# Optimization experiments

Hardware: AMD Instinct MI355X
Metric: run time of the kernel (lower is better)

Reference implementation:

```python
import jax, jax.numpy as jnp
import numpy as np

SCALE = 0.125  # 1/sqrt(d_k), d_k = 64


def setup_inputs() -> dict:
    key = jax.random.key(0)
    kq, kk, kv, kp = jax.random.split(key, 4)
    H, B, L, T, D = 16, 4, 1024, 1024, 64
    return {
        "query": jax.random.normal(kq, (H, B, L, D), dtype=jnp.float32),
        "key": jax.random.normal(kk, (H, B, T, D), dtype=jnp.float32),
        "value": jax.random.normal(kv, (H, B, T, D), dtype=jnp.float32),
        "prev_attention": jax.random.normal(kp, (H, B, L, T), dtype=jnp.float32),
    }


def reference(query, key, value, prev_attention):
    # scores: [h, b, l, t]
    scores = jnp.einsum("hblk,hbtk->hblt", query, key) * SCALE
    scores = scores + prev_attention
    attention = jax.nn.softmax(scores, axis=-1)
    # dropout disabled (rate 0.0) for deterministic reference
    output = jnp.einsum("hblt,hbtv->hblv", attention, value)
    return (output, attention)
```

## Files before the change

kernel.cpp:

```cpp
#include <hip/hip_runtime.h>

#define SCALE 0.125f

constexpr int L_ = 1024, T_ = 1024, D_ = 64, HB_ = 64;

using f32x4 = __attribute__((ext_vector_type(4))) float;
using half8 = __attribute__((ext_vector_type(8))) _Float16;
using half4 = __attribute__((ext_vector_type(4))) _Float16;

__global__ __launch_bounds__(256, 4) void zpass(
    const float* __restrict__ q, const float* __restrict__ kk,
    const float* __restrict__ prev, float* __restrict__ att,
    float* __restrict__ rz) {
  __shared__ __align__(16) _Float16 Ks[2][64][72];

  const int ltile = blockIdx.x, hb = blockIdx.y;
  const int tid = threadIdx.x;
  const int w = tid >> 6, l = tid & 63, l15 = l & 15, lg = l >> 4;
  const int qrow = ltile * 64 + w * 16 + l15;

  half8 qb[2];
  {
    const float* qp = q + ((size_t)hb * L_ + qrow) * D_ + lg * 8;
#pragma unroll
    for (int f = 0; f < 2; ++f)
#pragma unroll
      for (int e = 0; e < 8; ++e) qb[f][e] = (_Float16)qp[f * 32 + e];
  }

  const float* prow = prev + ((size_t)hb * L_ + qrow) * (size_t)T_;
  const float* kbase = kk + (size_t)hb * T_ * D_;
  _Float16* erow =
      (_Float16*)(att + ((size_t)hb * L_ + qrow) * (size_t)T_) + T_;

  const int sr = tid >> 2;
  const int sc = (tid & 3) * 16;

  float4 kreg[4];
  auto kload = [&](int t0) {
    const float* kp = kbase + (size_t)(t0 + sr) * D_ + sc;
#pragma unroll
    for (int p = 0; p < 4; ++p) kreg[p] = *(const float4*)(kp + p * 4);
  };
  auto kwrite = [&](int buf) {
#pragma unroll
    for (int p = 0; p < 4; ++p) {
      Ks[buf][sr][sc + p * 4 + 0] = (_Float16)kreg[p].x;
      Ks[buf][sr][sc + p * 4 + 1] = (_Float16)kreg[p].y;
      Ks[buf][sr][sc + p * 4 + 2] = (_Float16)kreg[p].z;
      Ks[buf][sr][sc + p * 4 + 3] = (_Float16)kreg[p].w;
    }
  };

  f32x4 pb[3][4];
  auto pload = [&](int c, int s) {
#pragma unroll
    for (int nt = 0; nt < 4; ++nt)
      pb[s][nt] = *(const f32x4*)(prow + c * 64 + nt * 16 + lg * 4);
  };

  kload(0);
  kwrite(0);
  pload(0, 0);
  pload(1, 1);

  float zsum = 0.f;

#pragma unroll
  for (int c = 0; c < 16; ++c) {
    const int cur = c & 1;
    if (c < 15) kload((c + 1) * 64);
    if (c < 14) pload(c + 2, (c + 2) % 3);
    __syncthreads();

#pragma unroll
    for (int nt = 0; nt < 4; ++nt) {
      half8 ka0 = *(const half8*)&Ks[cur][nt * 16 + l15][lg * 8];
      half8 ka1 = *(const half8*)&Ks[cur][nt * 16 + l15][32 + lg * 8];
      f32x4 acc = {0.f, 0.f, 0.f, 0.f};
      acc = __builtin_amdgcn_mfma_f32_16x16x32_f16(ka0, qb[0], acc, 0, 0, 0);
      acc = __builtin_amdgcn_mfma_f32_16x16x32_f16(ka1, qb[1], acc, 0, 0, 0);

      f32x4 pv = pb[c % 3][nt];
      float e0 = __expf(acc[0] * SCALE + pv[0]);
      float e1 = __expf(acc[1] * SCALE + pv[1]);
      float e2 = __expf(acc[2] * SCALE + pv[2]);
      float e3 = __expf(acc[3] * SCALE + pv[3]);
      zsum += (e0 + e1) + (e2 + e3);
      half4 ev;
      ev[0] = (_Float16)e0; ev[1] = (_Float16)e1;
      ev[2] = (_Float16)e2; ev[3] = (_Float16)e3;
      *(half4*)(erow + c * 64 + nt * 16 + lg * 4) = ev;
    }

    if (c < 15) kwrite(cur ^ 1);
  }

  zsum += __shfl_xor(zsum, 16, 64);
  zsum += __shfl_xor(zsum, 32, 64);
  if (lg == 0) rz[(size_t)hb * L_ + qrow] = 1.0f / zsum;
}

__global__ __launch_bounds__(256, 4) void pvpass(
    const float* __restrict__ vv, const float* __restrict__ rz,
    float* __restrict__ out, float* __restrict__ att) {
  __shared__ __align__(16) _Float16 Vt[2][64][72];

  const int ltile = blockIdx.x, hb = blockIdx.y;
  const int tid = threadIdx.x;
  const int w = tid >> 6, l = tid & 63, l15 = l & 15, lg = l >> 4;
  const int qrow = ltile * 64 + w * 16 + l15;

  const float rzq = rz[(size_t)hb * L_ + qrow];
  float* arow = att + ((size_t)hb * L_ + qrow) * (size_t)T_;
  const _Float16* erow = (const _Float16*)arow + T_;

  const float* vbase = vv + (size_t)hb * T_ * D_;
  const int sr = tid >> 2;
  const int dj = (tid & 3) * 4;

  float4 sv[4];
  auto stage_load = [&](int t0) {
    const float* vp = vbase + (size_t)(t0 + sr) * D_;
#pragma unroll
    for (int p = 0; p < 4; ++p) sv[p] = *(const float4*)(vp + p * 16 + dj);
  };
  auto stage_write = [&](int buf) {
#pragma unroll
    for (int p = 0; p < 4; ++p) {
      Vt[buf][p * 16 + dj + 0][sr] = (_Float16)sv[p].x;
      Vt[buf][p * 16 + dj + 1][sr] = (_Float16)sv[p].y;
      Vt[buf][p * 16 + dj + 2][sr] = (_Float16)sv[p].z;
      Vt[buf][p * 16 + dj + 3][sr] = (_Float16)sv[p].w;
    }
  };

  half8 eb[2][2];
  auto load_e = [&](int c, int buf) {
    eb[buf][0] = *(const half8*)(erow + c * 64 + lg * 8);
    eb[buf][1] = *(const half8*)(erow + c * 64 + 32 + lg * 8);
  };

  stage_load(0);
  stage_write(0);
  load_e(0, 0);

  f32x4 oacc[4];
#pragma unroll
  for (int nd = 0; nd < 4; ++nd) oacc[nd] = (f32x4){0.f, 0.f, 0.f, 0.f};

#pragma unroll
  for (int c = 0; c < 16; ++c) {
    __syncthreads();
    const int buf = c & 1;
    if (c < 15) {
      stage_load((c + 1) * 64);
      load_e(c + 1, (c + 1) & 1);
    }

    half8 af[2];
#pragma unroll
    for (int ks = 0; ks < 2; ++ks) {
      half8 ef = eb[buf][ks];
      f32x4 s0, s1;
#pragma unroll
      for (int e = 0; e < 4; ++e) {
        float v0 = (float)ef[e] * rzq;
        float v1 = (float)ef[4 + e] * rzq;
        s0[e] = v0; s1[e] = v1;
        af[ks][e] = (_Float16)v0;
        af[ks][4 + e] = (_Float16)v1;
      }
      *(f32x4*)(arow + c * 64 + ks * 32 + lg * 8) = s0;
      *(f32x4*)(arow + c * 64 + ks * 32 + lg * 8 + 4) = s1;
    }

#pragma unroll
    for (int ks = 0; ks < 2; ++ks)
#pragma unroll
      for (int nd = 0; nd < 4; ++nd) {
        half8 vb = *(const half8*)&Vt[buf][nd * 16 + l15][ks * 32 + lg * 8];
        oacc[nd] =
            __builtin_amdgcn_mfma_f32_16x16x32_f16(af[ks], vb, oacc[nd], 0, 0, 0);
      }

    if (c < 15) stage_write(buf ^ 1);
  }

  float* outw =
      out + ((size_t)hb * L_ + ltile * 64 + w * 16 + lg * 4) * (size_t)D_;
#pragma unroll
  for (int nd = 0; nd < 4; ++nd)
#pragma unroll
    for (int i = 0; i < 4; ++i)
      outw[(size_t)i * D_ + nd * 16 + l15] = oacc[nd][i];
}

extern "C" void kernel_launch(void* const* d_in, const int* in_sizes, int n_in,
                              void* d_out, int out_size, void* d_ws,
                              size_t ws_size, hipStream_t stream) {
  const float* q    = (const float*)d_in[0];
  const float* k    = (const float*)d_in[1];
  const float* v    = (const float*)d_in[2];
  const float* prev = (const float*)d_in[3];

  float* out = (float*)d_out;
  float* att = out + (size_t)HB_ * L_ * D_;
  float* rz  = (float*)d_ws;

  dim3 grid(L_ / 64, HB_);
  zpass<<<grid, 256, 0, stream>>>(q, k, prev, att, rz);
  pvpass<<<grid, 256, 0, stream>>>(v, rz, out, att);
}
```

Baseline: 254.8 us.

## Fuse score and PV passes into one kernel keeping exp values in LDS

Merges the two kernels into one. Unnormalized exp scores for a 32-row query tile are kept in 64KB of shared memory instead of being written as fp16 into the attention output buffer and read back. K and V are staged through a single swizzled LDS region, with each pair of waves splitting the key dimension and a final reduction across waves. This removes the global round trip of the intermediate exponentials and the row-sum workspace. In exchange it uses 80KB of LDS per block, which lowers occupancy, adds more barriers, and doubles K/V reloads because the query tile is smaller.

```diff
diff --git a/kernel.cpp b/kernel.cpp
--- a/kernel.cpp
+++ b/kernel.cpp
@@ -2,22 +2,37 @@
 
 #define SCALE 0.125f
 
-constexpr int L_ = 1024, T_ = 1024, D_ = 64, HB_ = 64;
+constexpr int L_ = 1024, T_ = 1024, D_ = 64, HB_ = 64, QB = 32;
 
 using f32x4 = __attribute__((ext_vector_type(4))) float;
 using half8 = __attribute__((ext_vector_type(8))) _Float16;
 using half4 = __attribute__((ext_vector_type(4))) _Float16;
 
-__global__ __launch_bounds__(256, 4) void zpass(
+__global__ __launch_bounds__(256, 2) void attn_fused(
     const float* __restrict__ q, const float* __restrict__ kk,
-    const float* __restrict__ prev, float* __restrict__ att,
-    float* __restrict__ rz) {
-  __shared__ __align__(16) _Float16 Ks[2][64][72];
-
-  const int ltile = blockIdx.x, hb = blockIdx.y;
+    const float* __restrict__ vv, const float* __restrict__ prev,
+    float* __restrict__ out, float* __restrict__ att) {
+  __shared__ __align__(16) unsigned char smem[81920];
+  unsigned char* Elb = smem;
+  unsigned char* KVb = smem + 65536;
+
+  const int ltile = blockIdx.x;
+  const int hb    = blockIdx.y;
   const int tid = threadIdx.x;
   const int w = tid >> 6, l = tid & 63, l15 = l & 15, lg = l >> 4;
-  const int qrow = ltile * 64 + w * 16 + l15;
+  const int rt = w >> 1, th = w & 1;
+  const int qloc = rt * 16 + l15;
+  const int qrow = ltile * QB + qloc;
+
+  auto elp = [&](int qq, int t) {
+    return Elb + qq * 2048 + (((unsigned)t * 2) ^ (((unsigned)qq & 7) << 4));
+  };
+  auto kp_ = [&](int row, int dbyte) {
+    return KVb + row * 128 + ((unsigned)dbyte ^ (((unsigned)row & 7) << 4));
+  };
+  auto vp_ = [&](int d, int tbyte) {
+    return KVb + d * 256 + ((unsigned)tbyte ^ (((unsigned)d & 7) << 4));
+  };
 
   half8 qb[2];
   {
@@ -28,60 +43,70 @@
       for (int e = 0; e < 8; ++e) qb[f][e] = (_Float16)qp[f * 32 + e];
   }
 
-  const float* prow = prev + ((size_t)hb * L_ + qrow) * (size_t)T_;
   const float* kbase = kk + (size_t)hb * T_ * D_;
-  _Float16* erow =
-      (_Float16*)(att + ((size_t)hb * L_ + qrow) * (size_t)T_) + T_;
-
-  const int sr = tid >> 2;
-  const int sc = (tid & 3) * 16;
-
-  float4 kreg[4];
-  auto kload = [&](int t0) {
-    const float* kp = kbase + (size_t)(t0 + sr) * D_ + sc;
-#pragma unroll
-    for (int p = 0; p < 4; ++p) kreg[p] = *(const float4*)(kp + p * 4);
-  };
-  auto kwrite = [&](int buf) {
-#pragma unroll
-    for (int p = 0; p < 4; ++p) {
-      Ks[buf][sr][sc + p * 4 + 0] = (_Float16)kreg[p].x;
-      Ks[buf][sr][sc + p * 4 + 1] = (_Float16)kreg[p].y;
-      Ks[buf][sr][sc + p * 4 + 2] = (_Float16)kreg[p].z;
-      Ks[buf][sr][sc + p * 4 + 3] = (_Float16)kreg[p].w;
-    }
-  };
-
-  f32x4 pb[3][4];
+  const float* vbase = vv + (size_t)hb * T_ * D_;
+  const float* prow  = prev + ((size_t)hb * L_ + qrow) * (size_t)T_;
+
+  const int sr = tid >> 1;
+  const int sh = (tid & 1) * 32;
+  float4 kreg[8];
+  auto gload = [&](const float* base, int c) {
+    const float* p = base + (size_t)(c * 128 + sr) * D_ + sh;
+#pragma unroll
+    for (int i = 0; i < 8; ++i) kreg[i] = *(const float4*)(p + i * 4);
+  };
+  auto kwrite = [&]() {
+#pragma unroll
+    for (int j = 0; j < 4; ++j) {
+      const float* f = (const float*)&kreg[j * 2];
+      half8 hv;
+#pragma unroll
+      for (int e = 0; e < 8; ++e) hv[e] = (_Float16)f[e];
+      *(half8*)kp_(sr, (sh + j * 8) * 2) = hv;
+    }
+  };
+  auto vwrite = [&]() {
+    const float* f = (const float*)kreg;
+#pragma unroll
+    for (int e = 0; e < 32; ++e)
+      *(_Float16*)vp_(sh + e, sr * 2) = (_Float16)f[e];
+  };
+
+  f32x4 pbuf[3][4];
   auto pload = [&](int c, int s) {
 #pragma unroll
     for (int nt = 0; nt < 4; ++nt)
-      pb[s][nt] = *(const f32x4*)(prow + c * 64 + nt * 16 + lg * 4);
-  };
-
-  kload(0);
-  kwrite(0);
+      pbuf[s][nt] =
+          *(const f32x4*)(prow + c * 128 + th * 64 + nt * 16 + lg * 4);
+  };
+
+  gload(kbase, 0);
+  kwrite();
   pload(0, 0);
   pload(1, 1);
 
   float zsum = 0.f;
 
 #pragma unroll
-  for (int c = 0; c < 16; ++c) {
-    const int cur = c & 1;
-    if (c < 15) kload((c + 1) * 64);
-    if (c < 14) pload(c + 2, (c + 2) % 3);
-    __syncthreads();
+  for (int c = 0; c < 8; ++c) {
+    __syncthreads();
+    if (c < 7) {
+      gload(kbase, c + 1);
+      if (c < 6) pload(c + 2, (c + 2) % 3);
+    } else {
+      gload(vbase, 0);
+    }
 
 #pragma unroll
     for (int nt = 0; nt < 4; ++nt) {
-      half8 ka0 = *(const half8*)&Ks[cur][nt * 16 + l15][lg * 8];
-      half8 ka1 = *(const half8*)&Ks[cur][nt * 16 + l15][32 + lg * 8];
+      const int trow = th * 64 + nt * 16 + l15;
+      half8 ka0 = *(const half8*)kp_(trow, lg * 16);
+      half8 ka1 = *(const half8*)kp_(trow, 64 + lg * 16);
       f32x4 acc = {0.f, 0.f, 0.f, 0.f};
       acc = __builtin_amdgcn_mfma_f32_16x16x32_f16(ka0, qb[0], acc, 0, 0, 0);
       acc = __builtin_amdgcn_mfma_f32_16x16x32_f16(ka1, qb[1], acc, 0, 0, 0);
 
-      f32x4 pv = pb[c % 3][nt];
+      f32x4 pv = pbuf[c % 3][nt];
       float e0 = __expf(acc[0] * SCALE + pv[0]);
       float e1 = __expf(acc[1] * SCALE + pv[1]);
       float e2 = __expf(acc[2] * SCALE + pv[2]);
@@ -90,110 +115,83 @@
       half4 ev;
       ev[0] = (_Float16)e0; ev[1] = (_Float16)e1;
       ev[2] = (_Float16)e2; ev[3] = (_Float16)e3;
-      *(half4*)(erow + c * 64 + nt * 16 + lg * 4) = ev;
-    }
-
-    if (c < 15) kwrite(cur ^ 1);
+      *(half4*)elp(qloc, c * 128 + th * 64 + nt * 16 + lg * 4) = ev;
+    }
+
+    __syncthreads();
+    if (c < 7) kwrite();
   }
 
   zsum += __shfl_xor(zsum, 16, 64);
   zsum += __shfl_xor(zsum, 32, 64);
-  if (lg == 0) rz[(size_t)hb * L_ + qrow] = 1.0f / zsum;
-}
-
-__global__ __launch_bounds__(256, 4) void pvpass(
-    const float* __restrict__ vv, const float* __restrict__ rz,
-    float* __restrict__ out, float* __restrict__ att) {
-  __shared__ __align__(16) _Float16 Vt[2][64][72];
-
-  const int ltile = blockIdx.x, hb = blockIdx.y;
-  const int tid = threadIdx.x;
-  const int w = tid >> 6, l = tid & 63, l15 = l & 15, lg = l >> 4;
-  const int qrow = ltile * 64 + w * 16 + l15;
-
-  const float rzq = rz[(size_t)hb * L_ + qrow];
-  float* arow = att + ((size_t)hb * L_ + qrow) * (size_t)T_;
-  const _Float16* erow = (const _Float16*)arow + T_;
-
-  const float* vbase = vv + (size_t)hb * T_ * D_;
-  const int sr = tid >> 2;
-  const int dj = (tid & 3) * 4;
-
-  float4 sv[4];
-  auto stage_load = [&](int t0) {
-    const float* vp = vbase + (size_t)(t0 + sr) * D_;
-#pragma unroll
-    for (int p = 0; p < 4; ++p) sv[p] = *(const float4*)(vp + p * 16 + dj);
-  };
-  auto stage_write = [&](int buf) {
-#pragma unroll
-    for (int p = 0; p < 4; ++p) {
-      Vt[buf][p * 16 + dj + 0][sr] = (_Float16)sv[p].x;
-      Vt[buf][p * 16 + dj + 1][sr] = (_Float16)sv[p].y;
-      Vt[buf][p * 16 + dj + 2][sr] = (_Float16)sv[p].z;
-      Vt[buf][p * 16 + dj + 3][sr] = (_Float16)sv[p].w;
-    }
-  };
-
-  half8 eb[2][2];
-  auto load_e = [&](int c, int buf) {
-    eb[buf][0] = *(const half8*)(erow + c * 64 + lg * 8);
-    eb[buf][1] = *(const half8*)(erow + c * 64 + 32 + lg * 8);
-  };
-
-  stage_load(0);
-  stage_write(0);
-  load_e(0, 0);
+  float* zb = (float*)KVb;
+  if (lg == 0) zb[w * 16 + l15] = zsum;
+  __syncthreads();
+  const float rzq = 1.0f / (zb[rt * 32 + l15] + zb[rt * 32 + 16 + l15]);
+  __syncthreads();
+  vwrite();
 
   f32x4 oacc[4];
 #pragma unroll
   for (int nd = 0; nd < 4; ++nd) oacc[nd] = (f32x4){0.f, 0.f, 0.f, 0.f};
 
-#pragma unroll
-  for (int c = 0; c < 16; ++c) {
-    __syncthreads();
-    const int buf = c & 1;
-    if (c < 15) {
-      stage_load((c + 1) * 64);
-      load_e(c + 1, (c + 1) & 1);
-    }
-
-    half8 af[2];
+  float* attw = att + ((size_t)hb * L_ + qrow) * (size_t)T_ + th * 64;
+
+#pragma unroll
+  for (int c = 0; c < 8; ++c) {
+    __syncthreads();
+    if (c < 7) gload(vbase, c + 1);
+
 #pragma unroll
     for (int ks = 0; ks < 2; ++ks) {
-      half8 ef = eb[buf][ks];
+      half8 ea =
+          *(const half8*)elp(qloc, c * 128 + th * 64 + ks * 32 + lg * 8);
       f32x4 s0, s1;
+      half8 af;
 #pragma unroll
       for (int e = 0; e < 4; ++e) {
-        float v0 = (float)ef[e] * rzq;
-        float v1 = (float)ef[4 + e] * rzq;
+        float v0 = (float)ea[e] * rzq;
+        float v1 = (float)ea[4 + e] * rzq;
         s0[e] = v0; s1[e] = v1;
-        af[ks][e] = (_Float16)v0;
-        af[ks][4 + e] = (_Float16)v1;
+        af[e] = (_Float16)v0;
+        af[4 + e] = (_Float16)v1;
       }
-      *(f32x4*)(arow + c * 64 + ks * 32 + lg * 8) = s0;
-      *(f32x4*)(arow + c * 64 + ks * 32 + lg * 8 + 4) = s1;
-    }
-
-#pragma unroll
-    for (int ks = 0; ks < 2; ++ks)
+      *(f32x4*)(attw + c * 128 + ks * 32 + lg * 8) = s0;
+      *(f32x4*)(attw + c * 128 + ks * 32 + lg * 8 + 4) = s1;
+
 #pragma unroll
       for (int nd = 0; nd < 4; ++nd) {
-        half8 vb = *(const half8*)&Vt[buf][nd * 16 + l15][ks * 32 + lg * 8];
+        half8 vb =
+            *(const half8*)vp_(nd * 16 + l15,
+                               (th * 64 + ks * 32 + lg * 8) * 2);
         oacc[nd] =
-            __builtin_amdgcn_mfma_f32_16x16x32_f16(af[ks], vb, oacc[nd], 0, 0, 0);
+            __builtin_amdgcn_mfma_f32_16x16x32_f16(af, vb, oacc[nd], 0, 0, 0);
       }
-
-    if (c < 15) stage_write(buf ^ 1);
-  }
-
-  float* outw =
-      out + ((size_t)hb * L_ + ltile * 64 + w * 16 + lg * 4) * (size_t)D_;
-#pragma unroll
-  for (int nd = 0; nd < 4; ++nd)
-#pragma unroll
-    for (int i = 0; i < 4; ++i)
-      outw[(size_t)i * D_ + nd * 16 + l15] = oacc[nd][i];
+    }
+
+    __syncthreads();
+    if (c < 7) vwrite();
+  }
+
+  float* ob = (float*)KVb;
+  if (th == 1) {
+#pragma unroll
+    for (int nd = 0; nd < 4; ++nd)
+#pragma unroll
+      for (int i = 0; i < 4; ++i)
+        ob[(rt * 16 + lg * 4 + i) * 64 + nd * 16 + l15] = oacc[nd][i];
+  }
+  __syncthreads();
+  if (th == 0) {
+    float* outw =
+        out + ((size_t)hb * L_ + ltile * QB + rt * 16 + lg * 4) * (size_t)D_;
+#pragma unroll
+    for (int nd = 0; nd < 4; ++nd)
+#pragma unroll
+      for (int i = 0; i < 4; ++i)
+        outw[(size_t)i * D_ + nd * 16 + l15] =
+            oacc[nd][i] + ob[(rt * 16 + lg * 4 + i) * 64 + nd * 16 + l15];
+  }
 }
 
 extern "C" void kernel_launch(void* const* d_in, const int* in_sizes, int n_in,
@@ -206,9 +204,7 @@
 
   float* out = (float*)d_out;
   float* att = out + (size_t)HB_ * L_ * D_;
-  float* rz  = (float*)d_ws;
-
-  dim3 grid(L_ / 64, HB_);
-  zpass<<<grid, 256, 0, stream>>>(q, k, prev, att, rz);
-  pvpass<<<grid, 256, 0, stream>>>(v, rz, out, att);
+
+  dim3 grid(L_ / QB, HB_);
+  attn_fused<<<grid, 256, 0, stream>>>(q, k, v, prev, out, att);
 }
```

Result: no change. 256.4 us (+0.6%).

## Pre-convert K and V to fp16 in workspace, restructure staging pipelines

Applied to the files above, without the earlier changes.

Adds two prepass kernels that convert K to fp16 and V to a transposed fp16 layout in the workspace, so the main kernels stream half the bytes and skip per-tile conversion and strided transposed LDS writes. The zpass and pvpass loops now prefetch two chunks ahead with a custom barrier, use partial unrolling, and raise the occupancy hint. The per-row reciprocal sum is stashed in the output buffer instead of the workspace. This adds two extra launches and a round trip of K/V through memory.

```diff
diff --git a/kernel.cpp b/kernel.cpp
--- a/kernel.cpp
+++ b/kernel.cpp
@@ -8,10 +8,52 @@
 using half8 = __attribute__((ext_vector_type(8))) _Float16;
 using half4 = __attribute__((ext_vector_type(4))) _Float16;
 
-__global__ __launch_bounds__(256, 4) void zpass(
-    const float* __restrict__ q, const float* __restrict__ kk,
-    const float* __restrict__ prev, float* __restrict__ att,
-    float* __restrict__ rz) {
+#define BARRIER() asm volatile("s_waitcnt lgkmcnt(0)\n\ts_barrier" ::: "memory")
+
+__global__ __launch_bounds__(256) void cvt_k(const float* __restrict__ k,
+                                             _Float16* __restrict__ kh) {
+  const size_t i = ((size_t)blockIdx.x * 256 + threadIdx.x) * 8;
+  f32x4 a = *(const f32x4*)(k + i);
+  f32x4 b = *(const f32x4*)(k + i + 4);
+  half8 h;
+#pragma unroll
+  for (int e = 0; e < 4; ++e) {
+    h[e] = (_Float16)a[e];
+    h[4 + e] = (_Float16)b[e];
+  }
+  *(half8*)(kh + i) = h;
+}
+
+__global__ __launch_bounds__(256) void cvt_v(const float* __restrict__ v,
+                                             _Float16* __restrict__ vh) {
+  __shared__ _Float16 ts[64][136];
+  const int tid = threadIdx.x;
+  const int hb = blockIdx.y;
+  const int t0 = blockIdx.x * 128;
+  {
+    const int tr = tid >> 1, dh = (tid & 1) * 32;
+    const float* p = v + ((size_t)hb * T_ + t0 + tr) * D_ + dh;
+#pragma unroll
+    for (int i = 0; i < 8; ++i) {
+      f32x4 r = *(const f32x4*)(p + i * 4);
+#pragma unroll
+      for (int e = 0; e < 4; ++e) ts[dh + i * 4 + e][tr] = (_Float16)r[e];
+    }
+  }
+  __syncthreads();
+  {
+    const int d = tid >> 2, tq = (tid & 3) * 32;
+    _Float16* qo = vh + ((size_t)hb * D_ + d) * T_ + t0 + tq;
+#pragma unroll
+    for (int i = 0; i < 4; ++i)
+      *(half8*)(qo + i * 8) = *(const half8*)&ts[d][tq + i * 8];
+  }
+}
+
+__global__ __launch_bounds__(256, 6) void zpass(
+    const float* __restrict__ q, const _Float16* __restrict__ Kh,
+    const float* __restrict__ prev, float* __restrict__ out,
+    float* __restrict__ att) {
   __shared__ __align__(16) _Float16 Ks[2][64][72];
 
   const int ltile = blockIdx.x, hb = blockIdx.y;
@@ -19,91 +61,84 @@
   const int w = tid >> 6, l = tid & 63, l15 = l & 15, lg = l >> 4;
   const int qrow = ltile * 64 + w * 16 + l15;
 
-  half8 qb[2];
+  half8 qb2[2];
   {
     const float* qp = q + ((size_t)hb * L_ + qrow) * D_ + lg * 8;
 #pragma unroll
     for (int f = 0; f < 2; ++f)
 #pragma unroll
-      for (int e = 0; e < 8; ++e) qb[f][e] = (_Float16)qp[f * 32 + e];
+      for (int e = 0; e < 8; ++e) qb2[f][e] = (_Float16)qp[f * 32 + e];
   }
 
   const float* prow = prev + ((size_t)hb * L_ + qrow) * (size_t)T_;
-  const float* kbase = kk + (size_t)hb * T_ * D_;
+  const _Float16* kb = Kh + (size_t)hb * T_ * D_;
   _Float16* erow =
       (_Float16*)(att + ((size_t)hb * L_ + qrow) * (size_t)T_) + T_;
 
-  const int sr = tid >> 2;
-  const int sc = (tid & 3) * 16;
-
-  float4 kreg[4];
-  auto kload = [&](int t0) {
-    const float* kp = kbase + (size_t)(t0 + sr) * D_ + sc;
-#pragma unroll
-    for (int p = 0; p < 4; ++p) kreg[p] = *(const float4*)(kp + p * 4);
-  };
-  auto kwrite = [&](int buf) {
-#pragma unroll
-    for (int p = 0; p < 4; ++p) {
-      Ks[buf][sr][sc + p * 4 + 0] = (_Float16)kreg[p].x;
-      Ks[buf][sr][sc + p * 4 + 1] = (_Float16)kreg[p].y;
-      Ks[buf][sr][sc + p * 4 + 2] = (_Float16)kreg[p].z;
-      Ks[buf][sr][sc + p * 4 + 3] = (_Float16)kreg[p].w;
-    }
-  };
-
-  f32x4 pb[3][4];
+  const int sr = tid >> 2, sc = (tid & 3) * 16;
+  half8 kst[2][2];
+  auto kload = [&](int c, int s) {
+    const _Float16* p = kb + (size_t)(c * 64 + sr) * D_ + sc;
+    kst[s][0] = *(const half8*)p;
+    kst[s][1] = *(const half8*)(p + 8);
+  };
+  auto kwrite = [&](int buf, int s) {
+    *(half8*)&Ks[buf][sr][sc] = kst[s][0];
+    *(half8*)&Ks[buf][sr][sc + 8] = kst[s][1];
+  };
+  f32x4 pb[2][4];
   auto pload = [&](int c, int s) {
 #pragma unroll
     for (int nt = 0; nt < 4; ++nt)
       pb[s][nt] = *(const f32x4*)(prow + c * 64 + nt * 16 + lg * 4);
   };
 
-  kload(0);
-  kwrite(0);
+  kload(0, 0);
   pload(0, 0);
+  kwrite(0, 0);
+  kload(1, 1);
   pload(1, 1);
 
   float zsum = 0.f;
 
-#pragma unroll
+#pragma unroll 4
   for (int c = 0; c < 16; ++c) {
-    const int cur = c & 1;
-    if (c < 15) kload((c + 1) * 64);
-    if (c < 14) pload(c + 2, (c + 2) % 3);
-    __syncthreads();
+    BARRIER();
+    f32x4 pvv[4];
+#pragma unroll
+    for (int nt = 0; nt < 4; ++nt) pvv[nt] = pb[c & 1][nt];
+    if (c < 14) { kload(c + 2, c & 1); pload(c + 2, c & 1); }
+    if (c < 15) kwrite((c + 1) & 1, (c + 1) & 1);
 
 #pragma unroll
     for (int nt = 0; nt < 4; ++nt) {
-      half8 ka0 = *(const half8*)&Ks[cur][nt * 16 + l15][lg * 8];
-      half8 ka1 = *(const half8*)&Ks[cur][nt * 16 + l15][32 + lg * 8];
+      const int trow = nt * 16 + l15;
+      half8 ka0 = *(const half8*)&Ks[c & 1][trow][lg * 8];
+      half8 ka1 = *(const half8*)&Ks[c & 1][trow][32 + lg * 8];
       f32x4 acc = {0.f, 0.f, 0.f, 0.f};
-      acc = __builtin_amdgcn_mfma_f32_16x16x32_f16(ka0, qb[0], acc, 0, 0, 0);
-      acc = __builtin_amdgcn_mfma_f32_16x16x32_f16(ka1, qb[1], acc, 0, 0, 0);
-
-      f32x4 pv = pb[c % 3][nt];
-      float e0 = __expf(acc[0] * SCALE + pv[0]);
-      float e1 = __expf(acc[1] * SCALE + pv[1]);
-      float e2 = __expf(acc[2] * SCALE + pv[2]);
-      float e3 = __expf(acc[3] * SCALE + pv[3]);
+      acc = __builtin_amdgcn_mfma_f32_16x16x32_f16(ka0, qb2[0], acc, 0, 0, 0);
+      acc = __builtin_amdgcn_mfma_f32_16x16x32_f16(ka1, qb2[1], acc, 0, 0, 0);
+
+      float e0 = __expf(acc[0] * SCALE + pvv[nt][0]);
+      float e1 = __expf(acc[1] * SCALE + pvv[nt][1]);
+      float e2 = __expf(acc[2] * SCALE + pvv[nt][2]);
+      float e3 = __expf(acc[3] * SCALE + pvv[nt][3]);
       zsum += (e0 + e1) + (e2 + e3);
       half4 ev;
       ev[0] = (_Float16)e0; ev[1] = (_Float16)e1;
       ev[2] = (_Float16)e2; ev[3] = (_Float16)e3;
       *(half4*)(erow + c * 64 + nt * 16 + lg * 4) = ev;
     }
-
-    if (c < 15) kwrite(cur ^ 1);
   }
 
   zsum += __shfl_xor(zsum, 16, 64);
   zsum += __shfl_xor(zsum, 32, 64);
-  if (lg == 0) rz[(size_t)hb * L_ + qrow] = 1.0f / zsum;
-}
-
-__global__ __launch_bounds__(256, 4) void pvpass(
-    const float* __restrict__ vv, const float* __restrict__ rz,
-    float* __restrict__ out, float* __restrict__ att) {
+  if (lg == 0) out[((size_t)hb * L_ + qrow) * (size_t)D_] = 1.0f / zsum;
+}
+
+__global__ __launch_bounds__(256, 6) void pvpass(
+    const _Float16* __restrict__ Vh, float* __restrict__ out,
+    float* __restrict__ att) {
   __shared__ __align__(16) _Float16 Vt[2][64][72];
 
   const int ltile = blockIdx.x, hb = blockIdx.y;
@@ -111,80 +146,68 @@
   const int w = tid >> 6, l = tid & 63, l15 = l & 15, lg = l >> 4;
   const int qrow = ltile * 64 + w * 16 + l15;
 
-  const float rzq = rz[(size_t)hb * L_ + qrow];
   float* arow = att + ((size_t)hb * L_ + qrow) * (size_t)T_;
   const _Float16* erow = (const _Float16*)arow + T_;
-
-  const float* vbase = vv + (size_t)hb * T_ * D_;
-  const int sr = tid >> 2;
-  const int dj = (tid & 3) * 4;
-
-  float4 sv[4];
-  auto stage_load = [&](int t0) {
-    const float* vp = vbase + (size_t)(t0 + sr) * D_;
-#pragma unroll
-    for (int p = 0; p < 4; ++p) sv[p] = *(const float4*)(vp + p * 16 + dj);
-  };
-  auto stage_write = [&](int buf) {
-#pragma unroll
-    for (int p = 0; p < 4; ++p) {
-      Vt[buf][p * 16 + dj + 0][sr] = (_Float16)sv[p].x;
-      Vt[buf][p * 16 + dj + 1][sr] = (_Float16)sv[p].y;
-      Vt[buf][p * 16 + dj + 2][sr] = (_Float16)sv[p].z;
-      Vt[buf][p * 16 + dj + 3][sr] = (_Float16)sv[p].w;
-    }
-  };
-
+  const float rzq = out[((size_t)hb * L_ + qrow) * (size_t)D_];
+  const _Float16* vbh = Vh + (size_t)hb * D_ * T_;
+
+  const int sr = tid >> 2, sc = (tid & 3) * 16;
+  half8 vst[2][2];
+  auto vload = [&](int c, int s) {
+    const _Float16* p = vbh + (size_t)sr * T_ + c * 64 + sc;
+    vst[s][0] = *(const half8*)p;
+    vst[s][1] = *(const half8*)(p + 8);
+  };
+  auto vwrite = [&](int buf, int s) {
+    *(half8*)&Vt[buf][sr][sc] = vst[s][0];
+    *(half8*)&Vt[buf][sr][sc + 8] = vst[s][1];
+  };
   half8 eb[2][2];
-  auto load_e = [&](int c, int buf) {
-    eb[buf][0] = *(const half8*)(erow + c * 64 + lg * 8);
-    eb[buf][1] = *(const half8*)(erow + c * 64 + 32 + lg * 8);
-  };
-
-  stage_load(0);
-  stage_write(0);
-  load_e(0, 0);
+  auto eload = [&](int c, int s) {
+    eb[s][0] = *(const half8*)(erow + c * 64 + lg * 8);
+    eb[s][1] = *(const half8*)(erow + c * 64 + 32 + lg * 8);
+  };
+
+  vload(0, 0);
+  eload(0, 0);
+  vwrite(0, 0);
+  vload(1, 1);
+  eload(1, 1);
 
   f32x4 oacc[4];
 #pragma unroll
   for (int nd = 0; nd < 4; ++nd) oacc[nd] = (f32x4){0.f, 0.f, 0.f, 0.f};
 
-#pragma unroll
+#pragma unroll 4
   for (int c = 0; c < 16; ++c) {
-    __syncthreads();
-    const int buf = c & 1;
-    if (c < 15) {
-      stage_load((c + 1) * 64);
-      load_e(c + 1, (c + 1) & 1);
-    }
-
-    half8 af[2];
+    BARRIER();
+    half8 e0 = eb[c & 1][0], e1 = eb[c & 1][1];
+    if (c < 14) { vload(c + 2, c & 1); eload(c + 2, c & 1); }
+    if (c < 15) vwrite((c + 1) & 1, (c + 1) & 1);
+
 #pragma unroll
     for (int ks = 0; ks < 2; ++ks) {
-      half8 ef = eb[buf][ks];
+      half8 ef = ks ? e1 : e0;
       f32x4 s0, s1;
+      half8 af;
 #pragma unroll
       for (int e = 0; e < 4; ++e) {
         float v0 = (float)ef[e] * rzq;
         float v1 = (float)ef[4 + e] * rzq;
         s0[e] = v0; s1[e] = v1;
-        af[ks][e] = (_Float16)v0;
-        af[ks][4 + e] = (_Float16)v1;
+        af[e] = (_Float16)v0;
+        af[4 + e] = (_Float16)v1;
       }
       *(f32x4*)(arow + c * 64 + ks * 32 + lg * 8) = s0;
       *(f32x4*)(arow + c * 64 + ks * 32 + lg * 8 + 4) = s1;
+
+#pragma unroll
+      for (int nd = 0; nd < 4; ++nd) {
+        half8 vb = *(const half8*)&Vt[c & 1][nd * 16 + l15][ks * 32 + lg * 8];
+        oacc[nd] =
+            __builtin_amdgcn_mfma_f32_16x16x32_f16(af, vb, oacc[nd], 0, 0, 0);
+      }
     }
-
-#pragma unroll
-    for (int ks = 0; ks < 2; ++ks)
-#pragma unroll
-      for (int nd = 0; nd < 4; ++nd) {
-        half8 vb = *(const half8*)&Vt[buf][nd * 16 + l15][ks * 32 + lg * 8];
-        oacc[nd] =
-            __builtin_amdgcn_mfma_f32_16x16x32_f16(af[ks], vb, oacc[nd], 0, 0, 0);
-      }
-
-    if (c < 15) stage_write(buf ^ 1);
   }
 
   float* outw =
@@ -206,9 +229,15 @@
 
   float* out = (float*)d_out;
   float* att = out + (size_t)HB_ * L_ * D_;
-  float* rz  = (float*)d_ws;
+
+  const size_t KV_ELEMS = (size_t)HB_ * T_ * D_;
+  _Float16* Kh = (_Float16*)d_ws;
+  _Float16* Vh = Kh + KV_ELEMS;
+
+  cvt_k<<<(int)(KV_ELEMS / (256 * 8)), 256, 0, stream>>>(k, Kh);
+  cvt_v<<<dim3(T_ / 128, HB_), 256, 0, stream>>>(v, Vh);
 
   dim3 grid(L_ / 64, HB_);
-  zpass<<<grid, 256, 0, stream>>>(q, k, prev, att, rz);
-  pvpass<<<grid, 256, 0, stream>>>(v, rz, out, att);
-}
+  zpass<<<grid, 256, 0, stream>>>(q, Kh, prev, out, att);
+  pvpass<<<grid, 256, 0, stream>>>(Vh, out, att);
+}
```

After: 389.4 us. 52.8% more time.
